# Kernel optimization log

Measured on AMD Instinct MI355X. Metric: run time of the kernel, lower is better.

Reference implementation:

```python
import jax, jax.numpy as jnp
import numpy as np

N_NODES = 100000
N_EDGES = 800000
D_IN = 128
D_HID = 128
N_CLASSES = 64


def _glorot(key, shape):
    fan_in, fan_out = shape[0], shape[1]
    lim = jnp.sqrt(6.0 / (fan_in + fan_out)).astype(jnp.float32)
    return jax.random.uniform(key, shape, jnp.float32, -lim, lim)


def setup_inputs() -> dict:
    key = jax.random.key(0)
    ks = jax.random.split(key, 20)
    inp = {
        "x": jax.random.normal(ks[0], (N_NODES, D_IN), jnp.float32),
        "edge_src": jax.random.randint(ks[1], (N_EDGES,), 0, N_NODES, jnp.int32),
        "edge_dst": jax.random.randint(ks[2], (N_EDGES,), 0, N_NODES, jnp.int32),
    }
    dims = [(D_IN, D_HID), (D_HID, D_HID), (D_HID, N_CLASSES)]
    k = 3
    for i, (di, do) in enumerate(dims):
        inp[f"Wp{i}"] = _glorot(ks[k], (di, di)); k += 1   # fc_pool: d_in -> d_in
        inp[f"bp{i}"] = jnp.zeros((di,), jnp.float32)
        inp[f"Ws{i}"] = _glorot(ks[k], (di, do)); k += 1   # fc_self (no bias)
        inp[f"Wn{i}"] = _glorot(ks[k], (di, do)); k += 1   # fc_neigh
        inp[f"bn{i}"] = jnp.zeros((do,), jnp.float32)
    return inp


def _sage_pool_layer(x, src, dst, Wp, bp, Ws, Wn, bn):
    # pool aggregator: max over in-edges of relu(fc_pool(h_src))
    m = jax.nn.relu(x @ Wp + bp)                 # [N, d_in]
    msg = m[src]                                 # [E, d_in] gather
    agg = jax.ops.segment_max(msg, dst, num_segments=N_NODES)  # scatter-max
    agg = jnp.where(jnp.isfinite(agg), agg, 0.0)  # zero-in-degree nodes -> 0
    return x @ Ws + agg @ Wn + bn


def reference(x, edge_src, edge_dst,
              Wp0, bp0, Ws0, Wn0, bn0,
              Wp1, bp1, Ws1, Wn1, bn1,
              Wp2, bp2, Ws2, Wn2, bn2):
    layers = [
        (Wp0, bp0, Ws0, Wn0, bn0),
        (Wp1, bp1, Ws1, Wn1, bn1),
        (Wp2, bp2, Ws2, Wn2, bn2),
    ]
    h = x
    for (Wp, bp, Ws, Wn, bn) in layers:
        # SAGEConv internal activation=relu followed by wrapper F.relu (idempotent)
        h = jax.nn.relu(_sage_pool_layer(h, edge_src, edge_dst, Wp, bp, Ws, Wn, bn))
    return jax.nn.log_softmax(h, axis=-1)
```

## Files before the change

kernel.cpp:

```cpp
#include <hip/hip_runtime.h>
#include <cstddef>
#include <cstdint>

#define NNODES 100000
#define NEDGES 800000
#define CAP 32
#define NXCD 8

typedef unsigned short u16;
typedef __attribute__((ext_vector_type(8))) short short8;
typedef __attribute__((ext_vector_type(8))) _Float16 half8;
typedef __attribute__((ext_vector_type(4))) float f32x4;
typedef __attribute__((ext_vector_type(4))) int int4v;

__device__ __forceinline__ u16 f32_to_bf16(float f) {
    union { float f; uint32_t u; } v; v.f = f;
    uint32_t r = v.u + 0x7FFF + ((v.u >> 16) & 1);
    return (u16)(r >> 16);
}
__device__ __forceinline__ u16 f32_to_f16(float f) {
    union { _Float16 h; u16 u; } v; v.h = (_Float16)f;
    return v.u;
}
__device__ __forceinline__ uint32_t pkmax(uint32_t a, uint32_t b) {
    uint32_t lo = max(a & 0xFFFFu, b & 0xFFFFu);
    uint32_t hi = max(a >> 16, b >> 16);
    return lo | (hi << 16);
}

__global__ __launch_bounds__(256) void zero_kernel(float4* __restrict__ p, int n4) {
    int i = blockIdx.x * blockDim.x + threadIdx.x;
    const int stride = gridDim.x * blockDim.x;
    for (; i < n4; i += stride) p[i] = make_float4(0.f, 0.f, 0.f, 0.f);
}

__global__ __launch_bounds__(256) void fill_bucket_kernel(
    const int* __restrict__ src, const int4v* __restrict__ dst4,
    int* __restrict__ deg, int* __restrict__ col2, int E4)
{
    const int xcd  = blockIdx.x & (NXCD - 1);
    const int grp  = blockIdx.x >> 3;
    const int ngrp = gridDim.x >> 3;
    const int lo = xcd * (NNODES / NXCD);
    const int hi = lo + (NNODES / NXCD);

    for (int i = grp * 256 + threadIdx.x; i < E4; i += ngrp * 256) {
        const int4v d4 = __builtin_nontemporal_load(&dst4[i]);
        const int e = i * 4;
#pragma unroll
        for (int j = 0; j < 4; ++j) {
            const int d = d4[j];
            if (d >= lo && d < hi) {
                const int r = atomicAdd(&deg[d], 1);
                if (r < CAP)
                    col2[d * CAP + r] = __builtin_nontemporal_load(&src[e + j]);
            }
        }
    }
}

__global__ __launch_bounds__(256) void bf16_cast_kernel(
    const float4* __restrict__ in, uint2* __restrict__ out, int n4)
{
    int i = blockIdx.x * 256 + threadIdx.x;
    const int stride = gridDim.x * 256;
    for (; i < n4; i += stride) {
        float4 v = in[i];
        out[i] = make_uint2(
            (uint32_t)f32_to_bf16(v.x) | ((uint32_t)f32_to_bf16(v.y) << 16),
            (uint32_t)f32_to_bf16(v.z) | ((uint32_t)f32_to_bf16(v.w) << 16));
    }
}

struct WPtrs { const float* w[9]; };

__global__ __launch_bounds__(256) void split_weights_kernel(WPtrs p, u16* __restrict__ wbase)
{
    const int idx = blockIdx.x * 256 + threadIdx.x;
    const int w = blockIdx.y;
    const int DO_ = (w >= 7) ? 64 : 128;
    if (idx >= 128 * DO_) return;
    const float v = p.w[w][idx];
    const int k = idx / DO_;
    const int c = idx - k * DO_;
    const bool use_f16 = (w == 2 || w == 5 || w == 8);
    wbase[w * 32768 + c * 128 + k] = use_f16 ? f32_to_f16(v) : f32_to_bf16(v);
}

__global__ __launch_bounds__(256) void copy_w_kernel(
    const uint32_t* __restrict__ w7, const uint32_t* __restrict__ w8,
    uint32_t* __restrict__ dstw)
{
    int i = blockIdx.x * 256 + threadIdx.x;
    if (i < 4096) dstw[i] = w7[i];
    else if (i < 8192) dstw[i] = w8[i - 4096];
}

template<int DO, bool DUAL, int OUT_MODE>
__global__ __launch_bounds__(512, 4) void mfma_gemm_kernel(
    const u16* __restrict__ A,
    const u16* __restrict__ Cq,
    const u16* __restrict__ WaT, const u16* __restrict__ WbT,
    const float* __restrict__ bias,
    float* __restrict__ outF, u16* __restrict__ outU,
    int N)
{
    constexpr int CT = DO / 16;
    constexpr int WS = 136;
    __shared__ u16 sW[(DUAL ? 2 : 1) * DO * WS];

    const int tid = threadIdx.x;

    for (int i = tid; i < DO * 16; i += 512) {
        const int r = i >> 4;
        const int c = (i & 15) << 3;
        *(short8*)&sW[r * WS + c] = *(const short8*)&WaT[r * 128 + c];
        if constexpr (DUAL)
            *(short8*)&sW[DO * WS + r * WS + c] = *(const short8*)&WbT[r * 128 + c];
    }

    const int lane = tid & 63;
    const int wid  = tid >> 6;
    const int l15  = lane & 15;
    const int lk   = (lane >> 4) << 3;
    const int row0 = blockIdx.x * 256 + wid * 32;

    int aoff0, aoff1;
    {
        int r0 = row0 + l15;      if (r0 > N - 1) r0 = N - 1;
        int r1 = row0 + 16 + l15; if (r1 > N - 1) r1 = N - 1;
        aoff0 = r0 * 128 + lk;
        aoff1 = r1 * 128 + lk;
    }

    f32x4 acc[2][CT];
#pragma unroll
    for (int m = 0; m < 2; ++m)
#pragma unroll
        for (int c = 0; c < CT; ++c) acc[m][c] = (f32x4){0.f, 0.f, 0.f, 0.f};

    __syncthreads();

#pragma unroll
    for (int k = 0; k < 4; ++k) {
        const int ko = 32 * k;
        short8 ah0 = *(const short8*)(A + aoff0 + ko);
        short8 ah1 = *(const short8*)(A + aoff1 + ko);
        half8 ch0, ch1;
        if constexpr (DUAL) {
            ch0 = *(const half8*)(Cq + aoff0 + ko);
            ch1 = *(const half8*)(Cq + aoff1 + ko);
        }
#pragma unroll
        for (int ct = 0; ct < CT; ++ct) {
            const int wb = (ct * 16 + l15) * WS + lk + ko;
            short8 wh = *(const short8*)&sW[wb];
            acc[0][ct] = __builtin_amdgcn_mfma_f32_16x16x32_bf16(ah0, wh, acc[0][ct], 0, 0, 0);
            acc[1][ct] = __builtin_amdgcn_mfma_f32_16x16x32_bf16(ah1, wh, acc[1][ct], 0, 0, 0);
            if constexpr (DUAL) {
                half8 vh = *(const half8*)&sW[DO * WS + wb];
                acc[0][ct] = __builtin_amdgcn_mfma_f32_16x16x32_f16(ch0, vh, acc[0][ct], 0, 0, 0);
                acc[1][ct] = __builtin_amdgcn_mfma_f32_16x16x32_f16(ch1, vh, acc[1][ct], 0, 0, 0);
            }
        }
    }

    float bv[CT];
#pragma unroll
    for (int ct = 0; ct < CT; ++ct) bv[ct] = bias[ct * 16 + l15];

    const int jrow = (lane >> 4) << 2;
#pragma unroll
    for (int m = 0; m < 2; ++m) {
#pragma unroll
        for (int j = 0; j < 4; ++j) {
            const int r = row0 + m * 16 + jrow + j;
            if constexpr (OUT_MODE == 3) {
                float v[CT];
                float mx = 0.f;
#pragma unroll
                for (int ct = 0; ct < CT; ++ct) {
                    v[ct] = fmaxf(acc[m][ct][j] + bv[ct], 0.f);
                    mx = fmaxf(mx, v[ct]);
                }
#pragma unroll
                for (int off = 1; off < 16; off <<= 1) mx = fmaxf(mx, __shfl_xor(mx, off));
                float s = 0.f;
#pragma unroll
                for (int ct = 0; ct < CT; ++ct) s += __expf(v[ct] - mx);
#pragma unroll
                for (int off = 1; off < 16; off <<= 1) s += __shfl_xor(s, off);
                const float lse = mx + __logf(s);
                if (r < N) {
#pragma unroll
                    for (int ct = 0; ct < CT; ++ct)
                        outF[(size_t)r * DO + ct * 16 + l15] = v[ct] - lse;
                }
            } else if (r < N) {
#pragma unroll
                for (int ct = 0; ct < CT; ++ct) {
                    float v = fmaxf(acc[m][ct][j] + bv[ct], 0.f);
                    const size_t o = (size_t)r * DO + ct * 16 + l15;
                    if constexpr (OUT_MODE == 0) {
                        outF[o] = v;
                    } else if constexpr (OUT_MODE == 1) {
                        outU[o] = f32_to_bf16(v);
                    } else if constexpr (OUT_MODE == 2) {
                        outU[o] = f32_to_f16(v);
                    }
                }
            }
        }
    }
}

__global__ __launch_bounds__(256) void aggregate_kernel(
    const uint4* __restrict__ m4,
    const int* __restrict__ deg,
    const int* __restrict__ col2,
    uint4* __restrict__ agg4, int N)
{
    const int tid  = threadIdx.x;
    const int l16  = tid & 15;
    const int node = (blockIdx.x * 256 + tid) >> 4;
    if (node >= N) return;
    int cnt = deg[node];
    if (cnt > CAP) cnt = CAP;
    const int base = node * CAP;

    uint32_t a0 = 0, a1 = 0, a2 = 0, a3 = 0;
    int e = 0;
    for (; e + 4 <= cnt; e += 4) {
        const int s0 = col2[base + e],     s1 = col2[base + e + 1];
        const int s2 = col2[base + e + 2], s3 = col2[base + e + 3];
        const uint4 v0 = m4[(size_t)s0 * 16 + l16];
        const uint4 v1 = m4[(size_t)s1 * 16 + l16];
        const uint4 v2 = m4[(size_t)s2 * 16 + l16];
        const uint4 v3 = m4[(size_t)s3 * 16 + l16];
        a0 = pkmax(a0, v0.x); a1 = pkmax(a1, v0.y); a2 = pkmax(a2, v0.z); a3 = pkmax(a3, v0.w);
        a0 = pkmax(a0, v1.x); a1 = pkmax(a1, v1.y); a2 = pkmax(a2, v1.z); a3 = pkmax(a3, v1.w);
        a0 = pkmax(a0, v2.x); a1 = pkmax(a1, v2.y); a2 = pkmax(a2, v2.z); a3 = pkmax(a3, v2.w);
        a0 = pkmax(a0, v3.x); a1 = pkmax(a1, v3.y); a2 = pkmax(a2, v3.z); a3 = pkmax(a3, v3.w);
    }
    for (; e < cnt; ++e) {
        const uint4 v0 = m4[(size_t)col2[base + e] * 16 + l16];
        a0 = pkmax(a0, v0.x); a1 = pkmax(a1, v0.y); a2 = pkmax(a2, v0.z); a3 = pkmax(a3, v0.w);
    }
    agg4[(size_t)node * 16 + l16] = make_uint4(a0, a1, a2, a3);
}

extern "C" void kernel_launch(void* const* d_in, const int* in_sizes, int n_in,
                              void* d_out, int out_size, void* d_ws, size_t ws_size,
                              hipStream_t stream)
{
    const int N = NNODES, E = NEDGES;
    const float* x  = (const float*)d_in[0];
    const int* esrc = (const int*)d_in[1];
    const int* edst = (const int*)d_in[2];
    const float* bp[3] = {(const float*)d_in[4], (const float*)d_in[9],  (const float*)d_in[14]};
    const float* bn[3] = {(const float*)d_in[7], (const float*)d_in[12], (const float*)d_in[17]};

    char* ws = (char*)d_ws;
    const size_t P = (size_t)N * 128 * 2;
    u16* p0 = (u16*)(ws);
    u16* p2 = (u16*)(ws + 2 * P);
    u16* p4 = (u16*)(ws + 4 * P);
    u16* p5 = (u16*)(ws + 5 * P);

    char* ob = (char*)d_out;
    int* deg    = (int*)ob;
    int* col2   = (int*)(ob + 409600);
    u16* wbase  = (u16*)(ob + 409600 + (size_t)N * CAP * 4);
    auto WT = [&](int i) { return wbase + i * 32768; };

    const int gblocks = (N + 255) / 256;
    const int ablocks = (N * 16 + 255) / 256;
    dim3 blk(256), gblk(512);

    zero_kernel<<<128, blk, 0, stream>>>((float4*)deg, N / 4);
    fill_bucket_kernel<<<2048, blk, 0, stream>>>(esrc, (const int4v*)edst, deg, col2, E / 4);

    WPtrs wp;
    wp.w[0] = (const float*)d_in[3];  wp.w[1] = (const float*)d_in[5];  wp.w[2] = (const float*)d_in[6];
    wp.w[3] = (const float*)d_in[8];  wp.w[4] = (const float*)d_in[10]; wp.w[5] = (const float*)d_in[11];
    wp.w[6] = (const float*)d_in[13]; wp.w[7] = (const float*)d_in[15]; wp.w[8] = (const float*)d_in[16];
    split_weights_kernel<<<dim3(64, 9), blk, 0, stream>>>(wp, wbase);
    bf16_cast_kernel<<<2048, blk, 0, stream>>>((const float4*)x, (uint2*)p0, N * 128 / 4);

    mfma_gemm_kernel<128, false, 2><<<gblocks, gblk, 0, stream>>>(
        p0, nullptr, WT(0), nullptr, bp[0], nullptr, p4, N);
    aggregate_kernel<<<ablocks, blk, 0, stream>>>((const uint4*)p4, deg, col2, (uint4*)p5, N);
    mfma_gemm_kernel<128, true, 1><<<gblocks, gblk, 0, stream>>>(
        p0, p5, WT(1), WT(2), bn[0], nullptr, p2, N);

    mfma_gemm_kernel<128, false, 2><<<gblocks, gblk, 0, stream>>>(
        p2, nullptr, WT(3), nullptr, bp[1], nullptr, p4, N);
    aggregate_kernel<<<ablocks, blk, 0, stream>>>((const uint4*)p4, deg, col2, (uint4*)p5, N);
    mfma_gemm_kernel<128, true, 1><<<gblocks, gblk, 0, stream>>>(
        p2, p5, WT(4), WT(5), bn[1], nullptr, p0, N);

    mfma_gemm_kernel<128, false, 2><<<gblocks, gblk, 0, stream>>>(
        p0, nullptr, WT(6), nullptr, bp[2], nullptr, p4, N);
    aggregate_kernel<<<ablocks, blk, 0, stream>>>((const uint4*)p4, deg, col2, (uint4*)p5, N);
    copy_w_kernel<<<32, blk, 0, stream>>>((const uint32_t*)WT(7), (const uint32_t*)WT(8), (uint32_t*)p4);
    mfma_gemm_kernel<64, true, 3><<<gblocks, gblk, 0, stream>>>(
        p0, p5, p4, p4 + 8192, bn[2], (float*)d_out, nullptr, N);
}
```

Baseline: 264.6 us.

## Pre-bin edges by destination partition before per-XCD bucket fill

Replaces the single bucket-fill pass, in which every XCD group scanned all edges and kept only its own destination range, with two passes. A binning kernel first sorts each 1024-edge chunk into 8 destination partitions in shared memory and appends them to global per-partition bins. A scatter kernel then has each XCD group read only its own bin and do the degree atomics and column writes. This removes the 8x redundant reads of the edge list in exchange for an extra kernel launch, extra global writes and reads of the bins, and a fixed bin capacity that silently drops edges if a partition overflows.

```diff
diff --git a/kernel.cpp b/kernel.cpp
--- a/kernel.cpp
+++ b/kernel.cpp
@@ -6,6 +6,8 @@
 #define NEDGES 800000
 #define CAP 32
 #define NXCD 8
+#define NPB (NNODES / NXCD)
+#define BINCAP 110592
 
 typedef unsigned short u16;
 typedef __attribute__((ext_vector_type(8))) short short8;
@@ -34,28 +36,78 @@
     for (; i < n4; i += stride) p[i] = make_float4(0.f, 0.f, 0.f, 0.f);
 }
 
-__global__ __launch_bounds__(256) void fill_bucket_kernel(
-    const int* __restrict__ src, const int4v* __restrict__ dst4,
-    int* __restrict__ deg, int* __restrict__ col2, int E4)
+__global__ __launch_bounds__(256) void bin_kernel(
+    const int* __restrict__ src, const int* __restrict__ dst,
+    int* __restrict__ gcnt, int* __restrict__ bind, int* __restrict__ bins, int E)
+{
+    __shared__ int ld[1024], ls[1024];
+    __shared__ int lcnt[8], lpre[8], lgb[8];
+    const int tid = threadIdx.x;
+    const int base = blockIdx.x * 1024;
+
+    if (tid < 8) lcnt[tid] = 0;
+    __syncthreads();
+
+    int d[4], s[4], slot[4], b[4];
+    int nv = 0;
+    if (base + tid * 4 + 3 < E) {
+        const int4v dd = *(const int4v*)&dst[base + tid * 4];
+        const int4v ss = *(const int4v*)&src[base + tid * 4];
+#pragma unroll
+        for (int j = 0; j < 4; ++j) { d[j] = dd[j]; s[j] = ss[j]; }
+        nv = 4;
+    } else {
+        for (int j = 0; j < 4; ++j) {
+            const int idx = base + tid * 4 + j;
+            if (idx < E) { d[nv] = dst[idx]; s[nv] = src[idx]; ++nv; }
+        }
+    }
+#pragma unroll 4
+    for (int j = 0; j < nv; ++j) {
+        b[j] = d[j] / NPB;
+        slot[j] = atomicAdd(&lcnt[b[j]], 1);
+    }
+    __syncthreads();
+    if (tid == 0) {
+        int run = 0;
+#pragma unroll
+        for (int k = 0; k < 8; ++k) { lpre[k] = run; run += lcnt[k]; }
+    }
+    __syncthreads();
+#pragma unroll 4
+    for (int j = 0; j < nv; ++j) {
+        const int p = lpre[b[j]] + slot[j];
+        ld[p] = d[j]; ls[p] = s[j];
+    }
+    if (tid < 8 && lcnt[tid] > 0) lgb[tid] = atomicAdd(&gcnt[tid], lcnt[tid]);
+    __syncthreads();
+    const int total = lpre[7] + lcnt[7];
+    for (int i = tid; i < total; i += 256) {
+        const int d_ = ld[i];
+        const int b_ = d_ / NPB;
+        const int g = lgb[b_] + (i - lpre[b_]);
+        if (g < BINCAP) {
+            bind[b_ * BINCAP + g] = d_;
+            bins[b_ * BINCAP + g] = ls[i];
+        }
+    }
+}
+
+__global__ __launch_bounds__(256) void scatter_fill_kernel(
+    const int* __restrict__ gcnt,
+    const int* __restrict__ bind, const int* __restrict__ bins,
+    int* __restrict__ deg, int* __restrict__ col2)
 {
     const int xcd  = blockIdx.x & (NXCD - 1);
     const int grp  = blockIdx.x >> 3;
     const int ngrp = gridDim.x >> 3;
-    const int lo = xcd * (NNODES / NXCD);
-    const int hi = lo + (NNODES / NXCD);
-
-    for (int i = grp * 256 + threadIdx.x; i < E4; i += ngrp * 256) {
-        const int4v d4 = __builtin_nontemporal_load(&dst4[i]);
-        const int e = i * 4;
-#pragma unroll
-        for (int j = 0; j < 4; ++j) {
-            const int d = d4[j];
-            if (d >= lo && d < hi) {
-                const int r = atomicAdd(&deg[d], 1);
-                if (r < CAP)
-                    col2[d * CAP + r] = __builtin_nontemporal_load(&src[e + j]);
-            }
-        }
+    int cnt = gcnt[xcd]; if (cnt > BINCAP) cnt = BINCAP;
+    const int* bd = bind + xcd * BINCAP;
+    const int* bs = bins + xcd * BINCAP;
+    for (int i = grp * 256 + threadIdx.x; i < cnt; i += ngrp * 256) {
+        const int d = bd[i];
+        const int r = atomicAdd(&deg[d], 1);
+        if (r < CAP) col2[d * CAP + r] = bs[i];
     }
 }
 
@@ -269,16 +321,21 @@
 
     char* ob = (char*)d_out;
     int* deg    = (int*)ob;
+    int* gcnt   = (int*)(ob + 400000);
     int* col2   = (int*)(ob + 409600);
     u16* wbase  = (u16*)(ob + 409600 + (size_t)N * CAP * 4);
+    int* bind   = (int*)(ob + 13800448);
+    int* bins   = (int*)(ob + 13800448 + 8 * BINCAP * 4);
     auto WT = [&](int i) { return wbase + i * 32768; };
 
     const int gblocks = (N + 255) / 256;
     const int ablocks = (N * 16 + 255) / 256;
+    const int bblocks = (E + 1023) / 1024;
     dim3 blk(256), gblk(512);
 
-    zero_kernel<<<128, blk, 0, stream>>>((float4*)deg, N / 4);
-    fill_bucket_kernel<<<2048, blk, 0, stream>>>(esrc, (const int4v*)edst, deg, col2, E / 4);
+    zero_kernel<<<128, blk, 0, stream>>>((float4*)ob, 409600 / 16);
+    bin_kernel<<<bblocks, blk, 0, stream>>>(esrc, edst, gcnt, bind, bins, E);
+    scatter_fill_kernel<<<2048, blk, 0, stream>>>(gcnt, bind, bins, deg, col2);
 
     WPtrs wp;
     wp.w[0] = (const float*)d_in[3];  wp.w[1] = (const float*)d_in[5];  wp.w[2] = (const float*)d_in[6];
```

After: 271.5 us. 2.6% more time.

## Fuse layer output GEMM with next layer's pool GEMM via shared-memory staging

Applied to the files above, without the earlier changes.

Adds a fused kernel that computes a layer's self+neighbour GEMM, writes the bf16 hidden output, stages it in shared memory, and immediately applies the next layer's pool projection. This removes two separate GEMM launches and their re-read of the hidden activations from global memory. The pool weights are read directly from global memory (cached) rather than shared memory. The graph buckets and weights move from the output buffer into workspace, which drops the final weight copy kernel.

```diff
diff --git a/kernel.cpp b/kernel.cpp
--- a/kernel.cpp
+++ b/kernel.cpp
@@ -85,133 +85,6 @@
     const int c = idx - k * DO_;
     const bool use_f16 = (w == 2 || w == 5 || w == 8);
     wbase[w * 32768 + c * 128 + k] = use_f16 ? f32_to_f16(v) : f32_to_bf16(v);
-}
-
-__global__ __launch_bounds__(256) void copy_w_kernel(
-    const uint32_t* __restrict__ w7, const uint32_t* __restrict__ w8,
-    uint32_t* __restrict__ dstw)
-{
-    int i = blockIdx.x * 256 + threadIdx.x;
-    if (i < 4096) dstw[i] = w7[i];
-    else if (i < 8192) dstw[i] = w8[i - 4096];
-}
-
-template<int DO, bool DUAL, int OUT_MODE>
-__global__ __launch_bounds__(512, 4) void mfma_gemm_kernel(
-    const u16* __restrict__ A,
-    const u16* __restrict__ Cq,
-    const u16* __restrict__ WaT, const u16* __restrict__ WbT,
-    const float* __restrict__ bias,
-    float* __restrict__ outF, u16* __restrict__ outU,
-    int N)
-{
-    constexpr int CT = DO / 16;
-    constexpr int WS = 136;
-    __shared__ u16 sW[(DUAL ? 2 : 1) * DO * WS];
-
-    const int tid = threadIdx.x;
-
-    for (int i = tid; i < DO * 16; i += 512) {
-        const int r = i >> 4;
-        const int c = (i & 15) << 3;
-        *(short8*)&sW[r * WS + c] = *(const short8*)&WaT[r * 128 + c];
-        if constexpr (DUAL)
-            *(short8*)&sW[DO * WS + r * WS + c] = *(const short8*)&WbT[r * 128 + c];
-    }
-
-    const int lane = tid & 63;
-    const int wid  = tid >> 6;
-    const int l15  = lane & 15;
-    const int lk   = (lane >> 4) << 3;
-    const int row0 = blockIdx.x * 256 + wid * 32;
-
-    int aoff0, aoff1;
-    {
-        int r0 = row0 + l15;      if (r0 > N - 1) r0 = N - 1;
-        int r1 = row0 + 16 + l15; if (r1 > N - 1) r1 = N - 1;
-        aoff0 = r0 * 128 + lk;
-        aoff1 = r1 * 128 + lk;
-    }
-
-    f32x4 acc[2][CT];
-#pragma unroll
-    for (int m = 0; m < 2; ++m)
-#pragma unroll
-        for (int c = 0; c < CT; ++c) acc[m][c] = (f32x4){0.f, 0.f, 0.f, 0.f};
-
-    __syncthreads();
-
-#pragma unroll
-    for (int k = 0; k < 4; ++k) {
-        const int ko = 32 * k;
-        short8 ah0 = *(const short8*)(A + aoff0 + ko);
-        short8 ah1 = *(const short8*)(A + aoff1 + ko);
-        half8 ch0, ch1;
-        if constexpr (DUAL) {
-            ch0 = *(const half8*)(Cq + aoff0 + ko);
-            ch1 = *(const half8*)(Cq + aoff1 + ko);
-        }
-#pragma unroll
-        for (int ct = 0; ct < CT; ++ct) {
-            const int wb = (ct * 16 + l15) * WS + lk + ko;
-            short8 wh = *(const short8*)&sW[wb];
-            acc[0][ct] = __builtin_amdgcn_mfma_f32_16x16x32_bf16(ah0, wh, acc[0][ct], 0, 0, 0);
-            acc[1][ct] = __builtin_amdgcn_mfma_f32_16x16x32_bf16(ah1, wh, acc[1][ct], 0, 0, 0);
-            if constexpr (DUAL) {
-                half8 vh = *(const half8*)&sW[DO * WS + wb];
-                acc[0][ct] = __builtin_amdgcn_mfma_f32_16x16x32_f16(ch0, vh, acc[0][ct], 0, 0, 0);
-                acc[1][ct] = __builtin_amdgcn_mfma_f32_16x16x32_f16(ch1, vh, acc[1][ct], 0, 0, 0);
-            }
-        }
-    }
-
-    float bv[CT];
-#pragma unroll
-    for (int ct = 0; ct < CT; ++ct) bv[ct] = bias[ct * 16 + l15];
-
-    const int jrow = (lane >> 4) << 2;
-#pragma unroll
-    for (int m = 0; m < 2; ++m) {
-#pragma unroll
-        for (int j = 0; j < 4; ++j) {
-            const int r = row0 + m * 16 + jrow + j;
-            if constexpr (OUT_MODE == 3) {
-                float v[CT];
-                float mx = 0.f;
-#pragma unroll
-                for (int ct = 0; ct < CT; ++ct) {
-                    v[ct] = fmaxf(acc[m][ct][j] + bv[ct], 0.f);
-                    mx = fmaxf(mx, v[ct]);
-                }
-#pragma unroll
-                for (int off = 1; off < 16; off <<= 1) mx = fmaxf(mx, __shfl_xor(mx, off));
-                float s = 0.f;
-#pragma unroll
-                for (int ct = 0; ct < CT; ++ct) s += __expf(v[ct] - mx);
-#pragma unroll
-                for (int off = 1; off < 16; off <<= 1) s += __shfl_xor(s, off);
-                const float lse = mx + __logf(s);
-                if (r < N) {
-#pragma unroll
-                    for (int ct = 0; ct < CT; ++ct)
-                        outF[(size_t)r * DO + ct * 16 + l15] = v[ct] - lse;
-                }
-            } else if (r < N) {
-#pragma unroll
-                for (int ct = 0; ct < CT; ++ct) {
-                    float v = fmaxf(acc[m][ct][j] + bv[ct], 0.f);
-                    const size_t o = (size_t)r * DO + ct * 16 + l15;
-                    if constexpr (OUT_MODE == 0) {
-                        outF[o] = v;
-                    } else if constexpr (OUT_MODE == 1) {
-                        outU[o] = f32_to_bf16(v);
-                    } else if constexpr (OUT_MODE == 2) {
-                        outU[o] = f32_to_f16(v);
-                    }
-                }
-            }
-        }
-    }
 }
 
 __global__ __launch_bounds__(256) void aggregate_kernel(
@@ -249,6 +122,244 @@
     agg4[(size_t)node * 16 + l16] = make_uint4(a0, a1, a2, a3);
 }
 
+template<int DO, bool DUAL, int OUT_MODE>
+__global__ __launch_bounds__(512, 4) void mfma_gemm_kernel(
+    const u16* __restrict__ A,
+    const u16* __restrict__ Cq,
+    const u16* __restrict__ WaT, const u16* __restrict__ WbT,
+    const float* __restrict__ bias,
+    float* __restrict__ outF, u16* __restrict__ outU, int N)
+{
+    constexpr int CT = DO / 16;
+    constexpr int WS = 136;
+    __shared__ u16 sW[(DUAL ? 2 : 1) * DO * WS];
+
+    const int tid = threadIdx.x;
+    for (int i = tid; i < DO * 16; i += 512) {
+        const int r = i >> 4;
+        const int c = (i & 15) << 3;
+        *(short8*)&sW[r * WS + c] = *(const short8*)&WaT[r * 128 + c];
+        if constexpr (DUAL)
+            *(short8*)&sW[DO * WS + r * WS + c] = *(const short8*)&WbT[r * 128 + c];
+    }
+
+    const int lane = tid & 63;
+    const int wid  = tid >> 6;
+    const int l15  = lane & 15;
+    const int sec  = lane >> 4;
+    const int lk   = sec << 3;
+    const int row0 = blockIdx.x * 256 + wid * 32;
+
+    int aoff0, aoff1;
+    {
+        int r0 = row0 + l15;      if (r0 > N - 1) r0 = N - 1;
+        int r1 = row0 + 16 + l15; if (r1 > N - 1) r1 = N - 1;
+        aoff0 = r0 * 128 + lk;
+        aoff1 = r1 * 128 + lk;
+    }
+
+    f32x4 acc[2][CT];
+#pragma unroll
+    for (int m = 0; m < 2; ++m)
+#pragma unroll
+        for (int c = 0; c < CT; ++c) acc[m][c] = (f32x4){0.f, 0.f, 0.f, 0.f};
+
+    __syncthreads();
+
+#pragma unroll
+    for (int k = 0; k < 4; ++k) {
+        const int ko = 32 * k;
+        short8 ah0 = *(const short8*)(A + aoff0 + ko);
+        short8 ah1 = *(const short8*)(A + aoff1 + ko);
+        half8 ch0, ch1;
+        if constexpr (DUAL) {
+            ch0 = *(const half8*)(Cq + aoff0 + ko);
+            ch1 = *(const half8*)(Cq + aoff1 + ko);
+        }
+#pragma unroll
+        for (int ct = 0; ct < CT; ++ct) {
+            const int wb = (ct * 16 + l15) * WS + lk + ko;
+            short8 wh = *(const short8*)&sW[wb];
+            acc[0][ct] = __builtin_amdgcn_mfma_f32_16x16x32_bf16(ah0, wh, acc[0][ct], 0, 0, 0);
+            acc[1][ct] = __builtin_amdgcn_mfma_f32_16x16x32_bf16(ah1, wh, acc[1][ct], 0, 0, 0);
+            if constexpr (DUAL) {
+                half8 vh = *(const half8*)&sW[DO * WS + wb];
+                acc[0][ct] = __builtin_amdgcn_mfma_f32_16x16x32_f16(ch0, vh, acc[0][ct], 0, 0, 0);
+                acc[1][ct] = __builtin_amdgcn_mfma_f32_16x16x32_f16(ch1, vh, acc[1][ct], 0, 0, 0);
+            }
+        }
+    }
+
+    float bv[CT];
+#pragma unroll
+    for (int ct = 0; ct < CT; ++ct) bv[ct] = bias[ct * 16 + l15];
+
+    const int jrow = sec << 2;
+#pragma unroll
+    for (int m = 0; m < 2; ++m) {
+#pragma unroll
+        for (int j = 0; j < 4; ++j) {
+            const int r = row0 + m * 16 + jrow + j;
+            if constexpr (OUT_MODE == 3) {
+                float v[CT];
+                float mx = 0.f;
+#pragma unroll
+                for (int ct = 0; ct < CT; ++ct) {
+                    v[ct] = fmaxf(acc[m][ct][j] + bv[ct], 0.f);
+                    mx = fmaxf(mx, v[ct]);
+                }
+#pragma unroll
+                for (int off = 1; off < 16; off <<= 1) mx = fmaxf(mx, __shfl_xor(mx, off));
+                float s = 0.f;
+#pragma unroll
+                for (int ct = 0; ct < CT; ++ct) s += __expf(v[ct] - mx);
+#pragma unroll
+                for (int off = 1; off < 16; off <<= 1) s += __shfl_xor(s, off);
+                const float lse = mx + __logf(s);
+                if (r < N) {
+#pragma unroll
+                    for (int ct = 0; ct < CT; ++ct)
+                        outF[(size_t)r * DO + ct * 16 + l15] = v[ct] - lse;
+                }
+            } else if (r < N) {
+#pragma unroll
+                for (int ct = 0; ct < CT; ++ct) {
+                    float v = fmaxf(acc[m][ct][j] + bv[ct], 0.f);
+                    const size_t o = (size_t)r * DO + ct * 16 + l15;
+                    if constexpr (OUT_MODE == 1) outU[o] = f32_to_bf16(v);
+                    else                          outU[o] = f32_to_f16(v);
+                }
+            }
+        }
+    }
+}
+
+__global__ __launch_bounds__(512, 4) void fused_dual_kernel(
+    const u16* __restrict__ A,
+    const u16* __restrict__ Cq,
+    const u16* __restrict__ WsT, const u16* __restrict__ WnT,
+    const float* __restrict__ bn_,
+    const u16* __restrict__ WpT, const float* __restrict__ bp_,
+    u16* __restrict__ outH, u16* __restrict__ outM, int N)
+{
+    constexpr int CT = 8;
+    constexpr int WS = 136;
+    __shared__ u16 sW[2 * 128 * WS];
+
+    const int tid = threadIdx.x;
+    for (int i = tid; i < 128 * 16; i += 512) {
+        const int r = i >> 4;
+        const int c = (i & 15) << 3;
+        *(short8*)&sW[r * WS + c] = *(const short8*)&WsT[r * 128 + c];
+        *(short8*)&sW[128 * WS + r * WS + c] = *(const short8*)&WnT[r * 128 + c];
+    }
+
+    const int lane = tid & 63;
+    const int wid  = tid >> 6;
+    const int l15  = lane & 15;
+    const int sec  = lane >> 4;
+    const int lk   = sec << 3;
+    const int row0 = blockIdx.x * 256 + wid * 32;
+
+    int aoff0, aoff1;
+    {
+        int r0 = row0 + l15;      if (r0 > N - 1) r0 = N - 1;
+        int r1 = row0 + 16 + l15; if (r1 > N - 1) r1 = N - 1;
+        aoff0 = r0 * 128 + lk;
+        aoff1 = r1 * 128 + lk;
+    }
+
+    f32x4 acc[2][CT];
+#pragma unroll
+    for (int m = 0; m < 2; ++m)
+#pragma unroll
+        for (int c = 0; c < CT; ++c) acc[m][c] = (f32x4){0.f, 0.f, 0.f, 0.f};
+
+    __syncthreads();
+
+#pragma unroll
+    for (int k = 0; k < 4; ++k) {
+        const int ko = 32 * k;
+        short8 ah0 = *(const short8*)(A + aoff0 + ko);
+        short8 ah1 = *(const short8*)(A + aoff1 + ko);
+        half8 ch0 = *(const half8*)(Cq + aoff0 + ko);
+        half8 ch1 = *(const half8*)(Cq + aoff1 + ko);
+#pragma unroll
+        for (int ct = 0; ct < CT; ++ct) {
+            const int wb = (ct * 16 + l15) * WS + lk + ko;
+            short8 wh = *(const short8*)&sW[wb];
+            half8 vh = *(const half8*)&sW[128 * WS + wb];
+            acc[0][ct] = __builtin_amdgcn_mfma_f32_16x16x32_bf16(ah0, wh, acc[0][ct], 0, 0, 0);
+            acc[1][ct] = __builtin_amdgcn_mfma_f32_16x16x32_bf16(ah1, wh, acc[1][ct], 0, 0, 0);
+            acc[0][ct] = __builtin_amdgcn_mfma_f32_16x16x32_f16(ch0, vh, acc[0][ct], 0, 0, 0);
+            acc[1][ct] = __builtin_amdgcn_mfma_f32_16x16x32_f16(ch1, vh, acc[1][ct], 0, 0, 0);
+        }
+    }
+
+    float bv[CT];
+#pragma unroll
+    for (int ct = 0; ct < CT; ++ct) bv[ct] = bn_[ct * 16 + l15];
+
+    const int jrow = sec << 2;
+
+    __syncthreads();
+
+#pragma unroll
+    for (int m = 0; m < 2; ++m) {
+#pragma unroll
+        for (int j = 0; j < 4; ++j) {
+            const int r  = row0 + m * 16 + jrow + j;
+            const int lr = wid * 32 + m * 16 + jrow + j;
+#pragma unroll
+            for (int ct = 0; ct < CT; ++ct) {
+                const float v = fmaxf(acc[m][ct][j] + bv[ct], 0.f);
+                const u16 hb = f32_to_bf16(v);
+                if (r < N) outH[(size_t)r * 128 + ct * 16 + l15] = hb;
+                sW[lr * WS + ct * 16 + l15] = hb;
+            }
+        }
+    }
+
+#pragma unroll
+    for (int m = 0; m < 2; ++m)
+#pragma unroll
+        for (int c = 0; c < CT; ++c) acc[m][c] = (f32x4){0.f, 0.f, 0.f, 0.f};
+
+    const int h0 = (wid * 32 + l15) * WS + lk;
+    const int h1 = (wid * 32 + 16 + l15) * WS + lk;
+#pragma unroll
+    for (int k = 0; k < 4; ++k) {
+        const int ko = 32 * k;
+        short8 ah0 = *(const short8*)&sW[h0 + ko];
+        short8 ah1 = *(const short8*)&sW[h1 + ko];
+#pragma unroll
+        for (int ct = 0; ct < CT; ++ct) {
+            short8 wp = *(const short8*)&WpT[(ct * 16 + l15) * 128 + lk + ko];
+            acc[0][ct] = __builtin_amdgcn_mfma_f32_16x16x32_bf16(ah0, wp, acc[0][ct], 0, 0, 0);
+            acc[1][ct] = __builtin_amdgcn_mfma_f32_16x16x32_bf16(ah1, wp, acc[1][ct], 0, 0, 0);
+        }
+    }
+
+    float bpv[CT];
+#pragma unroll
+    for (int ct = 0; ct < CT; ++ct) bpv[ct] = bp_[ct * 16 + l15];
+
+#pragma unroll
+    for (int m = 0; m < 2; ++m) {
+#pragma unroll
+        for (int j = 0; j < 4; ++j) {
+            const int r = row0 + m * 16 + jrow + j;
+            if (r < N) {
+#pragma unroll
+                for (int ct = 0; ct < CT; ++ct) {
+                    const float v = fmaxf(acc[m][ct][j] + bpv[ct], 0.f);
+                    outM[(size_t)r * 128 + ct * 16 + l15] = f32_to_f16(v);
+                }
+            }
+        }
+    }
+}
+
 extern "C" void kernel_launch(void* const* d_in, const int* in_sizes, int n_in,
                               void* d_out, int out_size, void* d_ws, size_t ws_size,
                               hipStream_t stream)
@@ -263,21 +374,21 @@
     char* ws = (char*)d_ws;
     const size_t P = (size_t)N * 128 * 2;
     u16* p0 = (u16*)(ws);
+    char* p1 = ws + P;
     u16* p2 = (u16*)(ws + 2 * P);
+    u16* wbase = (u16*)(ws + 3 * P);
     u16* p4 = (u16*)(ws + 4 * P);
     u16* p5 = (u16*)(ws + 5 * P);
 
-    char* ob = (char*)d_out;
-    int* deg    = (int*)ob;
-    int* col2   = (int*)(ob + 409600);
-    u16* wbase  = (u16*)(ob + 409600 + (size_t)N * CAP * 4);
+    int* deg  = (int*)p1;
+    int* col2 = (int*)(p1 + 409600);
     auto WT = [&](int i) { return wbase + i * 32768; };
 
-    const int gblocks = (N + 255) / 256;
+    const int gg = (N + 255) / 256;
     const int ablocks = (N * 16 + 255) / 256;
     dim3 blk(256), gblk(512);
 
-    zero_kernel<<<128, blk, 0, stream>>>((float4*)deg, N / 4);
+    zero_kernel<<<128, blk, 0, stream>>>((float4*)p1, 409600 / 16);
     fill_bucket_kernel<<<2048, blk, 0, stream>>>(esrc, (const int4v*)edst, deg, col2, E / 4);
 
     WPtrs wp;
@@ -287,22 +398,17 @@
     split_weights_kernel<<<dim3(64, 9), blk, 0, stream>>>(wp, wbase);
     bf16_cast_kernel<<<2048, blk, 0, stream>>>((const float4*)x, (uint2*)p0, N * 128 / 4);
 
-    mfma_gemm_kernel<128, false, 2><<<gblocks, gblk, 0, stream>>>(
+    mfma_gemm_kernel<128, false, 2><<<gg, gblk, 0, stream>>>(
         p0, nullptr, WT(0), nullptr, bp[0], nullptr, p4, N);
     aggregate_kernel<<<ablocks, blk, 0, stream>>>((const uint4*)p4, deg, col2, (uint4*)p5, N);
-    mfma_gemm_kernel<128, true, 1><<<gblocks, gblk, 0, stream>>>(
-        p0, p5, WT(1), WT(2), bn[0], nullptr, p2, N);
-
-    mfma_gemm_kernel<128, false, 2><<<gblocks, gblk, 0, stream>>>(
-        p2, nullptr, WT(3), nullptr, bp[1], nullptr, p4, N);
+    fused_dual_kernel<<<gg, gblk, 0, stream>>>(
+        p0, p5, WT(1), WT(2), bn[0], WT(3), bp[1], p2, p4, N);
+
     aggregate_kernel<<<ablocks, blk, 0, stream>>>((const uint4*)p4, deg, col2, (uint4*)p5, N);
-    mfma_gemm_kernel<128, true, 1><<<gblocks, gblk, 0, stream>>>(
-        p2, p5, WT(4), WT(5), bn[1], nullptr, p0, N);
-
-    mfma_gemm_kernel<128, false, 2><<<gblocks, gblk, 0, stream>>>(
-        p0, nullptr, WT(6), nullptr, bp[2], nullptr, p4, N);
+    fused_dual_kernel<<<gg, gblk, 0, stream>>>(
+        p2, p5, WT(4), WT(5), bn[1], WT(6), bp[2], p0, p4, N);
+
     aggregate_kernel<<<ablocks, blk, 0, stream>>>((const uint4*)p4, deg, col2, (uint4*)p5, N);
-    copy_w_kernel<<<32, blk, 0, stream>>>((const uint32_t*)WT(7), (const uint32_t*)WT(8), (uint32_t*)p4);
-    mfma_gemm_kernel<64, true, 3><<<gblocks, gblk, 0, stream>>>(
-        p0, p5, p4, p4 + 8192, bn[2], (float*)d_out, nullptr, N);
-}
+    mfma_gemm_kernel<64, true, 3><<<gg, gblk, 0, stream>>>(
+        p0, p5, WT(7), WT(8), bn[2], (float*)d_out, nullptr, N);
+}
```

Result: slower. 278.9 us (+5.4%).
